# Kernel optimization log

Measured on AMD Instinct MI355X. Metric: run time of the kernel, lower is better.

Reference implementation:

```python
import jax, jax.numpy as jnp
import numpy as np

NUM_AGENTS = 256
HIDDEN = 1024
RANK = 32
LOG_ALPHA_INIT = -1.0
ALPHA_MAX = 5.0
LN_EPS = 1e-5


def setup_inputs() -> dict:
    key = jax.random.key(0)
    k_h, k_ids, k_u, k_v = jax.random.split(key, 4)
    scale = 1.0 / (RANK ** 0.5)
    h = jax.random.normal(k_h, (8192, HIDDEN), dtype=jnp.float32)
    agent_ids = jax.random.randint(k_ids, (8192,), 0, NUM_AGENTS)
    # per-agent fixed random projections (buffers in the original module)
    projection_u = jax.random.normal(k_u, (NUM_AGENTS, HIDDEN, RANK), dtype=jnp.float32) * scale
    projection_v = jax.random.normal(k_v, (NUM_AGENTS, RANK, HIDDEN), dtype=jnp.float32) * scale
    log_alpha = jnp.asarray(LOG_ALPHA_INIT, dtype=jnp.float32)
    ln_gamma = jnp.ones((HIDDEN,), dtype=jnp.float32)
    ln_beta = jnp.zeros((HIDDEN,), dtype=jnp.float32)
    return {
        "h": h,
        "log_alpha": log_alpha,
        "ln_gamma": ln_gamma,
        "ln_beta": ln_beta,
        "projection_u": projection_u,
        "projection_v": projection_v,
        "agent_ids": agent_ids,
    }


def reference(h, log_alpha, ln_gamma, ln_beta, projection_u, projection_v, agent_ids):
    ids = agent_ids % NUM_AGENTS  # [B]
    u = projection_u[ids]  # [B, H, R] gathered per token
    v = projection_v[ids]  # [B, R, H]
    intermediate = jnp.einsum('bh,bhr->br', h, u)      # [B, R]
    perturbation = jnp.einsum('br,brh->bh', intermediate, v)  # [B, H]
    alpha = jnp.minimum(jnp.exp(log_alpha), ALPHA_MAX)
    h_div = h + alpha * perturbation
    # LayerNorm over last dim (biased variance, eps=1e-5)
    mean = jnp.mean(h_div, axis=-1, keepdims=True)
    var = jnp.mean(jnp.square(h_div - mean), axis=-1, keepdims=True)
    h_div = (h_div - mean) * jax.lax.rsqrt(var + LN_EPS) * ln_gamma + ln_beta
    return h_div
```

## Files before the change

kernel.cpp:

```cpp
#include <hip/hip_runtime.h>
#include <math.h>

#define NUM_AGENTS 256
#define HIDDEN 1024
#define RANK 32
#define NTOK 8192
#define TBATCH 8
#define MAXPER 128
#define REGCAP 256
#define ALPHA_MAX 5.0f
#define LN_EPS 1e-5f

typedef float f32x4 __attribute__((ext_vector_type(4)));

__global__ void zero_rc(int* __restrict__ rc) {
    if (threadIdx.x < 8) rc[threadIdx.x] = 0;
}

__global__ __launch_bounds__(256) void scan_kernel(
    const int* __restrict__ ids, int* __restrict__ rc, int* __restrict__ desc)
{
    __shared__ int toklist[MAXPER];
    __shared__ int cnt, basew;
    const int t = threadIdx.x;
    const int agent = blockIdx.x;
    if (t == 0) cnt = 0;
    __syncthreads();
    #pragma unroll
    for (int it = 0; it < NTOK / 1024; ++it) {
        int4 v = ((const int4*)ids)[t + 256 * it];
        int ib = 4 * (t + 256 * it);
        if ((v.x & (NUM_AGENTS - 1)) == agent) { int p = atomicAdd(&cnt, 1); if (p < MAXPER) toklist[p] = ib + 0; }
        if ((v.y & (NUM_AGENTS - 1)) == agent) { int p = atomicAdd(&cnt, 1); if (p < MAXPER) toklist[p] = ib + 1; }
        if ((v.z & (NUM_AGENTS - 1)) == agent) { int p = atomicAdd(&cnt, 1); if (p < MAXPER) toklist[p] = ib + 2; }
        if ((v.w & (NUM_AGENTS - 1)) == agent) { int p = atomicAdd(&cnt, 1); if (p < MAXPER) toklist[p] = ib + 3; }
    }
    __syncthreads();
    const int c = min(cnt, MAXPER);
    const int ng = (c + TBATCH - 1) / TBATCH;
    if (t == 0 && c > 0)
        basew = atomicAdd(&rc[agent & 7], ng);
    __syncthreads();
    if (t < ng) {
        int slot = basew + t;
        if (slot < REGCAP) {
            int* d = desc + ((size_t)(agent & 7) * REGCAP + slot) * 16;
            d[0] = agent;
            d[1] = min(TBATCH, c - t * TBATCH);
            #pragma unroll
            for (int m = 0; m < TBATCH; ++m)
                d[2 + m] = toklist[min(t * TBATCH + m, c - 1)];
        }
    }
}

__global__ __launch_bounds__(256) void div_inject_kernel(
    const float* __restrict__ hglob,
    const float* __restrict__ log_alpha,
    const float* __restrict__ gamma,
    const float* __restrict__ beta,
    const float* __restrict__ U,
    const float* __restrict__ V,
    const int* __restrict__ rc,
    const int* __restrict__ desc,
    float* __restrict__ out)
{
    __shared__ __align__(16) float Hs[TBATCH][HIDDEN];
    float* red0  = &Hs[0][0];
    float* inter = red0;
    float* wred  = red0 + 256;

    const int t = threadIdx.x;
    const int region = blockIdx.x & 7;
    const int slot = blockIdx.x >> 3;

    const int rcnt = min(rc[region], REGCAP);
    if (slot >= rcnt) return;

    const int* dsc = desc + ((size_t)region * REGCAP + slot) * 16;
    const int a  = dsc[0];
    const int nm = dsc[1];
    int tk[TBATCH];
    #pragma unroll
    for (int m = 0; m < TBATCH; ++m) tk[m] = dsc[2 + m];

    const float* Ua = U + (size_t)a * (HIDDEN * RANK);
    const float* Va = V + (size_t)a * (RANK * HIDDEN);

    const int r4 = (t & 7) * 4;
    const int kg = t >> 3;
    const int c  = t * 4;
    const int wave = t >> 6, lane = t & 63;

    float4 ub[2][4];
    #pragma unroll
    for (int i = 0; i < 4; ++i)
        ub[0][i] = *(const float4*)(Ua + (kg * 4 + i) * RANK + r4);

    const float alpha = fminf(__expf(log_alpha[0]), ALPHA_MAX);

    f32x4 h0v;
    {
        f32x4 hv[TBATCH];
        #pragma unroll
        for (int m = 0; m < TBATCH; ++m)
            hv[m] = __builtin_nontemporal_load((const f32x4*)(hglob + (size_t)tk[m] * HIDDEN + c));
        h0v = hv[0];
        #pragma unroll
        for (int m = 0; m < TBATCH; ++m)
            *(f32x4*)(&Hs[m][c]) = hv[m];
    }
    __syncthreads();

    float4 acc[TBATCH];
    #pragma unroll
    for (int m = 0; m < TBATCH; ++m) acc[m] = make_float4(0.f, 0.f, 0.f, 0.f);
    #pragma unroll
    for (int jb = 0; jb < 8; ++jb) {
        const int cur = jb & 1;
        if (jb < 7) {
            #pragma unroll
            for (int i = 0; i < 4; ++i)
                ub[cur ^ 1][i] = *(const float4*)(Ua + (kg * 4 + i + 128 * (jb + 1)) * RANK + r4);
        }
        const int hb = kg * 4 + 128 * jb;
        #pragma unroll
        for (int m = 0; m < TBATCH; ++m) {
            f32x4 h4 = *(const f32x4*)(&Hs[m][hb]);
            acc[m].x += h4.x * ub[cur][0].x + h4.y * ub[cur][1].x + h4.z * ub[cur][2].x + h4.w * ub[cur][3].x;
            acc[m].y += h4.x * ub[cur][0].y + h4.y * ub[cur][1].y + h4.z * ub[cur][2].y + h4.w * ub[cur][3].y;
            acc[m].z += h4.x * ub[cur][0].z + h4.y * ub[cur][1].z + h4.z * ub[cur][2].z + h4.w * ub[cur][3].z;
            acc[m].w += h4.x * ub[cur][0].w + h4.y * ub[cur][1].w + h4.z * ub[cur][2].w + h4.w * ub[cur][3].w;
        }
    }
    #pragma unroll
    for (int off = 8; off <= 32; off <<= 1) {
        #pragma unroll
        for (int m = 0; m < TBATCH; ++m) {
            acc[m].x += __shfl_xor(acc[m].x, off, 64);
            acc[m].y += __shfl_xor(acc[m].y, off, 64);
            acc[m].z += __shfl_xor(acc[m].z, off, 64);
            acc[m].w += __shfl_xor(acc[m].w, off, 64);
        }
    }
    __syncthreads();
    if (lane < 8) {
        #pragma unroll
        for (int m = 0; m < TBATCH; ++m)
            *(float4*)(&red0[wave * 256 + m * 32 + r4]) = acc[m];
    }

    float4 vb[2][4];
    #pragma unroll
    for (int j = 0; j < 4; ++j)
        vb[0][j] = *(const float4*)(Va + j * HIDDEN + c);

    __syncthreads();
    {
        int m = t >> 5, rr = t & 31;
        inter[m * 32 + rr] = red0[m * 32 + rr] + red0[256 + m * 32 + rr]
                           + red0[512 + m * 32 + rr] + red0[768 + m * 32 + rr];
    }
    __syncthreads();

    float4 p[TBATCH];
    #pragma unroll
    for (int m = 0; m < TBATCH; ++m) p[m] = make_float4(0.f, 0.f, 0.f, 0.f);
    #pragma unroll
    for (int rb = 0; rb < 8; ++rb) {
        const int cur = rb & 1;
        if (rb < 7) {
            #pragma unroll
            for (int j = 0; j < 4; ++j)
                vb[cur ^ 1][j] = *(const float4*)(Va + (4 * (rb + 1) + j) * HIDDEN + c);
        }
        #pragma unroll
        for (int m = 0; m < TBATCH; ++m) {
            f32x4 iq = *(const f32x4*)(&inter[m * 32 + rb * 4]);
            p[m].x += iq.x * vb[cur][0].x + iq.y * vb[cur][1].x + iq.z * vb[cur][2].x + iq.w * vb[cur][3].x;
            p[m].y += iq.x * vb[cur][0].y + iq.y * vb[cur][1].y + iq.z * vb[cur][2].y + iq.w * vb[cur][3].y;
            p[m].z += iq.x * vb[cur][0].z + iq.y * vb[cur][1].z + iq.z * vb[cur][2].z + iq.w * vb[cur][3].z;
            p[m].w += iq.x * vb[cur][0].w + iq.y * vb[cur][1].w + iq.z * vb[cur][2].w + iq.w * vb[cur][3].w;
        }
    }

    float s[TBATCH], q[TBATCH];
    #pragma unroll
    for (int m = 0; m < TBATCH; ++m) {
        f32x4 h4 = (m == 0) ? h0v : *(const f32x4*)(&Hs[m][c]);
        p[m].x = h4.x + alpha * p[m].x;
        p[m].y = h4.y + alpha * p[m].y;
        p[m].z = h4.z + alpha * p[m].z;
        p[m].w = h4.w + alpha * p[m].w;
        s[m] = p[m].x + p[m].y + p[m].z + p[m].w;
        q[m] = p[m].x * p[m].x + p[m].y * p[m].y + p[m].z * p[m].z + p[m].w * p[m].w;
    }
    #pragma unroll
    for (int off = 32; off > 0; off >>= 1) {
        #pragma unroll
        for (int m = 0; m < TBATCH; ++m) {
            s[m] += __shfl_xor(s[m], off, 64);
            q[m] += __shfl_xor(q[m], off, 64);
        }
    }
    if (lane == 0) {
        #pragma unroll
        for (int m = 0; m < TBATCH; ++m) {
            wred[wave * 16 + m] = s[m];
            wred[wave * 16 + 8 + m] = q[m];
        }
    }
    __syncthreads();

    const float4 gv = *(const float4*)(gamma + c);
    const float4 bv = *(const float4*)(beta + c);
    #pragma unroll
    for (int m = 0; m < TBATCH; ++m) {
        if (m < nm) {
            float S = wred[m] + wred[16 + m] + wred[32 + m] + wred[48 + m];
            float Q = wred[8 + m] + wred[24 + m] + wred[40 + m] + wred[56 + m];
            float mean = S * (1.0f / HIDDEN);
            float rstd = rsqrtf(Q * (1.0f / HIDDEN) - mean * mean + LN_EPS);
            f32x4 o;
            o.x = (p[m].x - mean) * rstd * gv.x + bv.x;
            o.y = (p[m].y - mean) * rstd * gv.y + bv.y;
            o.z = (p[m].z - mean) * rstd * gv.z + bv.z;
            o.w = (p[m].w - mean) * rstd * gv.w + bv.w;
            __builtin_nontemporal_store(o, (f32x4*)(out + (size_t)tk[m] * HIDDEN + c));
        }
    }
}

extern "C" void kernel_launch(void* const* d_in, const int* in_sizes, int n_in,
                              void* d_out, int out_size, void* d_ws, size_t ws_size,
                              hipStream_t stream) {
    const float* h     = (const float*)d_in[0];
    const float* la    = (const float*)d_in[1];
    const float* gamma = (const float*)d_in[2];
    const float* beta  = (const float*)d_in[3];
    const float* U     = (const float*)d_in[4];
    const float* V     = (const float*)d_in[5];
    const int* ids     = (const int*)d_in[6];
    float* out         = (float*)d_out;

    int* rc   = (int*)d_ws;
    int* desc = rc + 16;

    zero_rc<<<1, 64, 0, stream>>>(rc);
    scan_kernel<<<NUM_AGENTS, 256, 0, stream>>>(ids, rc, desc);
    div_inject_kernel<<<8 * REGCAP, 256, 0, stream>>>(
        h, la, gamma, beta, U, V, rc, desc, out);
}
```

Baseline: 206.3 us.

## Assign two tokens per wave and replace block barriers with wave shuffles

Restructures the inject kernel so each 64-lane wave handles two tokens end to end: it loads their hidden rows, computes the rank projection, does the V expansion, and applies LayerNorm using only intra-wave shuffles. All __syncthreads and LDS cross-wave reductions are removed. The cost is that each wave streams the full U and V slabs of the agent, which raises global and L2 load traffic per block and lowers arithmetic reuse per loaded U/V element.

```diff
diff --git a/kernel.cpp b/kernel.cpp
--- a/kernel.cpp
+++ b/kernel.cpp
@@ -66,9 +66,6 @@
     float* __restrict__ out)
 {
     __shared__ __align__(16) float Hs[TBATCH][HIDDEN];
-    float* red0  = &Hs[0][0];
-    float* inter = red0;
-    float* wred  = red0 + 256;
 
     const int t = threadIdx.x;
     const int region = blockIdx.x & 7;
@@ -80,153 +77,119 @@
     const int* dsc = desc + ((size_t)region * REGCAP + slot) * 16;
     const int a  = dsc[0];
     const int nm = dsc[1];
-    int tk[TBATCH];
-    #pragma unroll
-    for (int m = 0; m < TBATCH; ++m) tk[m] = dsc[2 + m];
+
+    const int w = t >> 6, l = t & 63;
+    const int m0 = 2 * w, m1 = 2 * w + 1;
+    const int tk0 = dsc[2 + m0];
+    const int tk1 = dsc[2 + m1];
 
     const float* Ua = U + (size_t)a * (HIDDEN * RANK);
     const float* Va = V + (size_t)a * (RANK * HIDDEN);
 
-    const int r4 = (t & 7) * 4;
-    const int kg = t >> 3;
-    const int c  = t * 4;
-    const int wave = t >> 6, lane = t & 63;
-
-    float4 ub[2][4];
-    #pragma unroll
-    for (int i = 0; i < 4; ++i)
-        ub[0][i] = *(const float4*)(Ua + (kg * 4 + i) * RANK + r4);
+    const int cq = l * 4;
+    const int r4 = (l & 7) * 4;
+    const int ks = l >> 3;
 
     const float alpha = fminf(__expf(log_alpha[0]), ALPHA_MAX);
 
-    f32x4 h0v;
-    {
-        f32x4 hv[TBATCH];
-        #pragma unroll
-        for (int m = 0; m < TBATCH; ++m)
-            hv[m] = __builtin_nontemporal_load((const f32x4*)(hglob + (size_t)tk[m] * HIDDEN + c));
-        h0v = hv[0];
-        #pragma unroll
-        for (int m = 0; m < TBATCH; ++m)
-            *(f32x4*)(&Hs[m][c]) = hv[m];
-    }
-    __syncthreads();
-
-    float4 acc[TBATCH];
-    #pragma unroll
-    for (int m = 0; m < TBATCH; ++m) acc[m] = make_float4(0.f, 0.f, 0.f, 0.f);
-    #pragma unroll
-    for (int jb = 0; jb < 8; ++jb) {
-        const int cur = jb & 1;
-        if (jb < 7) {
-            #pragma unroll
-            for (int i = 0; i < 4; ++i)
-                ub[cur ^ 1][i] = *(const float4*)(Ua + (kg * 4 + i + 128 * (jb + 1)) * RANK + r4);
-        }
-        const int hb = kg * 4 + 128 * jb;
-        #pragma unroll
-        for (int m = 0; m < TBATCH; ++m) {
-            f32x4 h4 = *(const f32x4*)(&Hs[m][hb]);
-            acc[m].x += h4.x * ub[cur][0].x + h4.y * ub[cur][1].x + h4.z * ub[cur][2].x + h4.w * ub[cur][3].x;
-            acc[m].y += h4.x * ub[cur][0].y + h4.y * ub[cur][1].y + h4.z * ub[cur][2].y + h4.w * ub[cur][3].y;
-            acc[m].z += h4.x * ub[cur][0].z + h4.y * ub[cur][1].z + h4.z * ub[cur][2].z + h4.w * ub[cur][3].z;
-            acc[m].w += h4.x * ub[cur][0].w + h4.y * ub[cur][1].w + h4.z * ub[cur][2].w + h4.w * ub[cur][3].w;
-        }
+    #pragma unroll
+    for (int k = 0; k < 4; ++k) {
+        *(f32x4*)(&Hs[m0][cq + 256 * k]) =
+            __builtin_nontemporal_load((const f32x4*)(hglob + (size_t)tk0 * HIDDEN + cq + 256 * k));
+        *(f32x4*)(&Hs[m1][cq + 256 * k]) =
+            __builtin_nontemporal_load((const f32x4*)(hglob + (size_t)tk1 * HIDDEN + cq + 256 * k));
+    }
+
+    float4 a0 = make_float4(0.f, 0.f, 0.f, 0.f);
+    float4 a1 = make_float4(0.f, 0.f, 0.f, 0.f);
+    #pragma unroll 8
+    for (int it = 0; it < 128; ++it) {
+        const int hh = ks + 8 * it;
+        float4 u = *(const float4*)(Ua + hh * RANK + r4);
+        float h0 = Hs[m0][hh];
+        float h1 = Hs[m1][hh];
+        a0.x += h0 * u.x; a0.y += h0 * u.y; a0.z += h0 * u.z; a0.w += h0 * u.w;
+        a1.x += h1 * u.x; a1.y += h1 * u.y; a1.z += h1 * u.z; a1.w += h1 * u.w;
     }
     #pragma unroll
     for (int off = 8; off <= 32; off <<= 1) {
-        #pragma unroll
-        for (int m = 0; m < TBATCH; ++m) {
-            acc[m].x += __shfl_xor(acc[m].x, off, 64);
-            acc[m].y += __shfl_xor(acc[m].y, off, 64);
-            acc[m].z += __shfl_xor(acc[m].z, off, 64);
-            acc[m].w += __shfl_xor(acc[m].w, off, 64);
-        }
-    }
-    __syncthreads();
-    if (lane < 8) {
-        #pragma unroll
-        for (int m = 0; m < TBATCH; ++m)
-            *(float4*)(&red0[wave * 256 + m * 32 + r4]) = acc[m];
-    }
-
-    float4 vb[2][4];
-    #pragma unroll
-    for (int j = 0; j < 4; ++j)
-        vb[0][j] = *(const float4*)(Va + j * HIDDEN + c);
-
-    __syncthreads();
-    {
-        int m = t >> 5, rr = t & 31;
-        inter[m * 32 + rr] = red0[m * 32 + rr] + red0[256 + m * 32 + rr]
-                           + red0[512 + m * 32 + rr] + red0[768 + m * 32 + rr];
-    }
-    __syncthreads();
-
-    float4 p[TBATCH];
-    #pragma unroll
-    for (int m = 0; m < TBATCH; ++m) p[m] = make_float4(0.f, 0.f, 0.f, 0.f);
+        a0.x += __shfl_xor(a0.x, off, 64); a0.y += __shfl_xor(a0.y, off, 64);
+        a0.z += __shfl_xor(a0.z, off, 64); a0.w += __shfl_xor(a0.w, off, 64);
+        a1.x += __shfl_xor(a1.x, off, 64); a1.y += __shfl_xor(a1.y, off, 64);
+        a1.z += __shfl_xor(a1.z, off, 64); a1.w += __shfl_xor(a1.w, off, 64);
+    }
+
+    float4 p0[4], p1[4];
+    #pragma unroll
+    for (int k = 0; k < 4; ++k) {
+        p0[k] = make_float4(0.f, 0.f, 0.f, 0.f);
+        p1[k] = make_float4(0.f, 0.f, 0.f, 0.f);
+    }
     #pragma unroll
     for (int rb = 0; rb < 8; ++rb) {
-        const int cur = rb & 1;
-        if (rb < 7) {
-            #pragma unroll
-            for (int j = 0; j < 4; ++j)
-                vb[cur ^ 1][j] = *(const float4*)(Va + (4 * (rb + 1) + j) * HIDDEN + c);
-        }
-        #pragma unroll
-        for (int m = 0; m < TBATCH; ++m) {
-            f32x4 iq = *(const f32x4*)(&inter[m * 32 + rb * 4]);
-            p[m].x += iq.x * vb[cur][0].x + iq.y * vb[cur][1].x + iq.z * vb[cur][2].x + iq.w * vb[cur][3].x;
-            p[m].y += iq.x * vb[cur][0].y + iq.y * vb[cur][1].y + iq.z * vb[cur][2].y + iq.w * vb[cur][3].y;
-            p[m].z += iq.x * vb[cur][0].z + iq.y * vb[cur][1].z + iq.z * vb[cur][2].z + iq.w * vb[cur][3].z;
-            p[m].w += iq.x * vb[cur][0].w + iq.y * vb[cur][1].w + iq.z * vb[cur][2].w + iq.w * vb[cur][3].w;
-        }
-    }
-
-    float s[TBATCH], q[TBATCH];
-    #pragma unroll
-    for (int m = 0; m < TBATCH; ++m) {
-        f32x4 h4 = (m == 0) ? h0v : *(const f32x4*)(&Hs[m][c]);
-        p[m].x = h4.x + alpha * p[m].x;
-        p[m].y = h4.y + alpha * p[m].y;
-        p[m].z = h4.z + alpha * p[m].z;
-        p[m].w = h4.w + alpha * p[m].w;
-        s[m] = p[m].x + p[m].y + p[m].z + p[m].w;
-        q[m] = p[m].x * p[m].x + p[m].y * p[m].y + p[m].z * p[m].z + p[m].w * p[m].w;
-    }
-    #pragma unroll
-    for (int off = 32; off > 0; off >>= 1) {
-        #pragma unroll
-        for (int m = 0; m < TBATCH; ++m) {
-            s[m] += __shfl_xor(s[m], off, 64);
-            q[m] += __shfl_xor(q[m], off, 64);
-        }
-    }
-    if (lane == 0) {
-        #pragma unroll
-        for (int m = 0; m < TBATCH; ++m) {
-            wred[wave * 16 + m] = s[m];
-            wred[wave * 16 + 8 + m] = q[m];
-        }
-    }
-    __syncthreads();
-
-    const float4 gv = *(const float4*)(gamma + c);
-    const float4 bv = *(const float4*)(beta + c);
-    #pragma unroll
-    for (int m = 0; m < TBATCH; ++m) {
-        if (m < nm) {
-            float S = wred[m] + wred[16 + m] + wred[32 + m] + wred[48 + m];
-            float Q = wred[8 + m] + wred[24 + m] + wred[40 + m] + wred[56 + m];
-            float mean = S * (1.0f / HIDDEN);
-            float rstd = rsqrtf(Q * (1.0f / HIDDEN) - mean * mean + LN_EPS);
+        float4 i0, i1;
+        i0.x = __shfl(a0.x, rb, 64); i0.y = __shfl(a0.y, rb, 64);
+        i0.z = __shfl(a0.z, rb, 64); i0.w = __shfl(a0.w, rb, 64);
+        i1.x = __shfl(a1.x, rb, 64); i1.y = __shfl(a1.y, rb, 64);
+        i1.z = __shfl(a1.z, rb, 64); i1.w = __shfl(a1.w, rb, 64);
+        const float* Vr = Va + (size_t)(rb * 4) * HIDDEN + cq;
+        #define PVSTEP(J, CM)                                                      \
+        {                                                                          \
+            _Pragma("unroll")                                                      \
+            for (int k = 0; k < 4; ++k) {                                          \
+                float4 v = *(const float4*)(Vr + (J) * HIDDEN + 256 * k);          \
+                p0[k].x += i0.CM * v.x; p0[k].y += i0.CM * v.y;                    \
+                p0[k].z += i0.CM * v.z; p0[k].w += i0.CM * v.w;                    \
+                p1[k].x += i1.CM * v.x; p1[k].y += i1.CM * v.y;                    \
+                p1[k].z += i1.CM * v.z; p1[k].w += i1.CM * v.w;                    \
+            }                                                                      \
+        }
+        PVSTEP(0, x) PVSTEP(1, y) PVSTEP(2, z) PVSTEP(3, w)
+        #undef PVSTEP
+    }
+
+    float s0 = 0.f, q0 = 0.f, s1 = 0.f, q1 = 0.f;
+    #pragma unroll
+    for (int k = 0; k < 4; ++k) {
+        f32x4 h40 = *(const f32x4*)(&Hs[m0][cq + 256 * k]);
+        f32x4 h41 = *(const f32x4*)(&Hs[m1][cq + 256 * k]);
+        p0[k].x = h40.x + alpha * p0[k].x; p0[k].y = h40.y + alpha * p0[k].y;
+        p0[k].z = h40.z + alpha * p0[k].z; p0[k].w = h40.w + alpha * p0[k].w;
+        p1[k].x = h41.x + alpha * p1[k].x; p1[k].y = h41.y + alpha * p1[k].y;
+        p1[k].z = h41.z + alpha * p1[k].z; p1[k].w = h41.w + alpha * p1[k].w;
+        s0 += p0[k].x + p0[k].y + p0[k].z + p0[k].w;
+        q0 += p0[k].x * p0[k].x + p0[k].y * p0[k].y + p0[k].z * p0[k].z + p0[k].w * p0[k].w;
+        s1 += p1[k].x + p1[k].y + p1[k].z + p1[k].w;
+        q1 += p1[k].x * p1[k].x + p1[k].y * p1[k].y + p1[k].z * p1[k].z + p1[k].w * p1[k].w;
+    }
+    #pragma unroll
+    for (int off = 1; off <= 32; off <<= 1) {
+        s0 += __shfl_xor(s0, off, 64); q0 += __shfl_xor(q0, off, 64);
+        s1 += __shfl_xor(s1, off, 64); q1 += __shfl_xor(q1, off, 64);
+    }
+    const float inv = 1.0f / HIDDEN;
+    const float mean0 = s0 * inv, rstd0 = rsqrtf(q0 * inv - mean0 * mean0 + LN_EPS);
+    const float mean1 = s1 * inv, rstd1 = rsqrtf(q1 * inv - mean1 * mean1 + LN_EPS);
+
+    #pragma unroll
+    for (int k = 0; k < 4; ++k) {
+        float4 gvk = *(const float4*)(gamma + cq + 256 * k);
+        float4 bvk = *(const float4*)(beta + cq + 256 * k);
+        if (m0 < nm) {
             f32x4 o;
-            o.x = (p[m].x - mean) * rstd * gv.x + bv.x;
-            o.y = (p[m].y - mean) * rstd * gv.y + bv.y;
-            o.z = (p[m].z - mean) * rstd * gv.z + bv.z;
-            o.w = (p[m].w - mean) * rstd * gv.w + bv.w;
-            __builtin_nontemporal_store(o, (f32x4*)(out + (size_t)tk[m] * HIDDEN + c));
+            o.x = (p0[k].x - mean0) * rstd0 * gvk.x + bvk.x;
+            o.y = (p0[k].y - mean0) * rstd0 * gvk.y + bvk.y;
+            o.z = (p0[k].z - mean0) * rstd0 * gvk.z + bvk.z;
+            o.w = (p0[k].w - mean0) * rstd0 * gvk.w + bvk.w;
+            __builtin_nontemporal_store(o, (f32x4*)(out + (size_t)tk0 * HIDDEN + cq + 256 * k));
+        }
+        if (m1 < nm) {
+            f32x4 o;
+            o.x = (p1[k].x - mean1) * rstd1 * gvk.x + bvk.x;
+            o.y = (p1[k].y - mean1) * rstd1 * gvk.y + bvk.y;
+            o.z = (p1[k].z - mean1) * rstd1 * gvk.z + bvk.z;
+            o.w = (p1[k].w - mean1) * rstd1 * gvk.w + bvk.w;
+            __builtin_nontemporal_store(o, (f32x4*)(out + (size_t)tk1 * HIDDEN + cq + 256 * k));
         }
     }
 }
```

Measured after the change: 209.7 us. No clear change (+1.6%).
